# Optimization experiments

Hardware: AMD Instinct MI355X
Metric: run time of the kernel (lower is better)

Reference implementation:

```python
import jax, jax.numpy as jnp
import numpy as np

ACT_BIT = 3
W_BIT = 2


def fake_quant(x, bits):
    """Symmetric uniform fake-quantization to `bits` bits (dequantized values)."""
    qmax = float((1 << (bits - 1)) - 1)
    scale = jnp.max(jnp.abs(x)) / qmax
    scale = jnp.where(scale == 0, jnp.ones_like(scale), scale)
    return jnp.clip(jnp.round(x / scale), -qmax, qmax) * scale


def setup_inputs() -> dict:
    key = jax.random.key(0)
    kA, kX, kWi, kWo = jax.random.split(key, 4)
    N, D_IN, D_H, D_OUT = 8192, 128, 64, 16
    A = jax.random.normal(kA, (N, N), dtype=jnp.float32)       # dense subgraph adjacency (binarized inside)
    X = jax.random.normal(kX, (N, D_IN), dtype=jnp.float32)    # node features
    W_in = jax.random.normal(kWi, (D_IN, D_H), dtype=jnp.float32)
    W_out = jax.random.normal(kWo, (D_H, D_OUT), dtype=jnp.float32)
    return {"A": A, "X": X, "W_in": W_in, "W_out": W_out}


def reference(A, X, W_in, W_out):
    # QGTC GCNConv_Qnt: A quantized to 1 bit, activations to act_bit, weights to w_bit.
    Aq = (A > 0).astype(A.dtype)                 # 1-bit adjacency (bit_qnt(A, 1))
    Xq = fake_quant(X, ACT_BIT)                  # X_Qnt
    Wi = fake_quant(W_in, W_BIT)                 # weight_Qnt
    Wo = fake_quant(W_out, W_BIT)
    # Layer 1: mm_v1(X, W_in) then mm_v1(A, .) with output re-quantized to act_bit
    h = Aq @ (Xq @ Wi)                           # [N, D_H]
    hq = fake_quant(h, ACT_BIT)
    # Layer 2 (output layer)
    out = Aq @ (hq @ Wo)                         # [N, D_OUT]
    return out
```

## Files before the change

### kernel.cpp

```cpp
#include <hip/hip_runtime.h>

#define NN 8192
#define DIN 128
#define DH 64
#define DOUT 16
#define KS 16

typedef _Float16 half8 __attribute__((ext_vector_type(8)));
typedef float f32x4 __attribute__((ext_vector_type(4)));

#define OFF_SC    0u
#define OFF_PART  256u
#define OFF_WIQ   2048u
#define OFF_WOQ   34816u
#define OFF_YT    65536u
#define OFF_RT    1114112u
#define OFF_HF    1376256u
#define OFF_BITS  3473408u
#define OFF_P1    11862016u
#define OFF_P2    45416448u

__device__ __forceinline__ float getscale(const unsigned* sc, int idx, float qmax) {
  float s = __uint_as_float(sc[idx]) / qmax;
  return (s == 0.0f) ? 1.0f : s;
}

__device__ __forceinline__ half8 expand8(unsigned bb) {
  uint4 w;
  w.x = ((bb & 1u)  ? 0x3C00u : 0u) | ((bb & 2u)   ? 0x3C000000u : 0u);
  w.y = ((bb & 4u)  ? 0x3C00u : 0u) | ((bb & 8u)   ? 0x3C000000u : 0u);
  w.z = ((bb & 16u) ? 0x3C00u : 0u) | ((bb & 32u)  ? 0x3C000000u : 0u);
  w.w = ((bb & 64u) ? 0x3C00u : 0u) | ((bb & 128u) ? 0x3C000000u : 0u);
  return __builtin_bit_cast(half8, w);
}

__global__ __launch_bounds__(256) void k_scales(const float* __restrict__ X,
                                                const float* __restrict__ Wi,
                                                const float* __restrict__ Wo,
                                                unsigned* part) {
  __shared__ float red[256];
  int t = threadIdx.x, b = blockIdx.x;
  float m = 0.0f;
  if (b < 240) {
    for (int i = b * 256 + t; i < NN * DIN; i += 240 * 256) m = fmaxf(m, fabsf(X[i]));
  } else if (b == 240) {
    for (int i = t; i < DIN * DH; i += 256) m = fmaxf(m, fabsf(Wi[i]));
  } else {
    for (int i = t; i < DH * DOUT; i += 256) m = fmaxf(m, fabsf(Wo[i]));
  }
  red[t] = m; __syncthreads();
  for (int s = 128; s > 0; s >>= 1) {
    if (t < s) red[t] = fmaxf(red[t], red[t + s]);
    __syncthreads();
  }
  if (t == 0) part[b] = __float_as_uint(red[0]);
}

__global__ __launch_bounds__(256) void k_quantW(const float* __restrict__ Wi,
                                                const float* __restrict__ Wo,
                                                const unsigned* __restrict__ part,
                                                unsigned* sc,
                                                float* __restrict__ Wiq,
                                                float* __restrict__ Woq) {
  __shared__ float red[256];
  int t = threadIdx.x;
  red[t] = (t < 240) ? __uint_as_float(part[t]) : 0.0f;
  __syncthreads();
  for (int s = 128; s > 0; s >>= 1) {
    if (t < s) red[t] = fmaxf(red[t], red[t + s]);
    __syncthreads();
  }
  if (t == 0) {
    sc[0] = __float_as_uint(red[0]);
    sc[1] = part[240];
    sc[2] = part[241];
    sc[3] = 0u;
  }
  float swi = __uint_as_float(part[240]); swi = (swi == 0.0f) ? 1.0f : swi;
  float swo = __uint_as_float(part[241]); swo = (swo == 0.0f) ? 1.0f : swo;
  for (int i = t; i < DIN * DH; i += 256) {
    float q = rintf(Wi[i] / swi);
    Wiq[i] = fminf(fmaxf(q, -1.0f), 1.0f);
  }
  for (int i = t; i < DH * DOUT; i += 256) {
    float q = rintf(Wo[i] / swo);
    Woq[i] = fminf(fmaxf(q, -1.0f), 1.0f);
  }
}

__global__ __launch_bounds__(256) void k_bitsY(const float* __restrict__ A,
                                               const float* __restrict__ X,
                                               const float* __restrict__ Wiq,
                                               const unsigned* __restrict__ sc,
                                               unsigned char* __restrict__ bits,
                                               _Float16* __restrict__ YT) {
  __shared__ float Xs[8][129];
  __shared__ float Ws[DIN][DH];
  const int t = threadIdx.x, bx = blockIdx.x;
  if (bx < 4096) {
    const int g = bx * 256 + t;
    const float4* ap = (const float4*)(A + (size_t)g * 64);
    float4 v[16];
#pragma unroll
    for (int u = 0; u < 16; ++u) v[u] = ap[u];
    unsigned lo = 0u, hi = 0u;
#pragma unroll
    for (int u = 0; u < 8; ++u) {
      lo |= ((unsigned)(v[u].x > 0.0f) << (4 * u + 0)) | ((unsigned)(v[u].y > 0.0f) << (4 * u + 1)) |
            ((unsigned)(v[u].z > 0.0f) << (4 * u + 2)) | ((unsigned)(v[u].w > 0.0f) << (4 * u + 3));
      float4 w = v[u + 8];
      hi |= ((unsigned)(w.x > 0.0f) << (4 * u + 0)) | ((unsigned)(w.y > 0.0f) << (4 * u + 1)) |
            ((unsigned)(w.z > 0.0f) << (4 * u + 2)) | ((unsigned)(w.w > 0.0f) << (4 * u + 3));
    }
    uint2 bw; bw.x = lo; bw.y = hi;
    *(uint2*)(bits + (size_t)g * 8) = bw;
    return;
  }
  float sx = getscale(sc, 0, 3.0f);
  const int by = bx - 4096;
  const int k0 = by * 8;
  for (int i = t; i < 8 * DIN; i += 256) {
    int r = i >> 7, c = i & 127;
    float q = rintf(X[(size_t)(k0 + r) * DIN + c] / sx);
    Xs[r][c] = fminf(fmaxf(q, -3.0f), 3.0f);
  }
  for (int i = t; i < DIN * DH; i += 256) Ws[i >> 6][i & 63] = Wiq[i];
  __syncthreads();
  const int r = t & 7, jp = t >> 3, j = jp * 2;
  float a0 = 0.0f, a1 = 0.0f;
  for (int n = 0; n < DIN; ++n) {
    float xv = Xs[r][n];
    a0 = fmaf(xv, Ws[n][j], a0);
    a1 = fmaf(xv, Ws[n][j + 1], a1);
  }
  YT[(size_t)j * NN + k0 + r]       = (_Float16)a0;
  YT[(size_t)(j + 1) * NN + k0 + r] = (_Float16)a1;
}

__global__ __launch_bounds__(256) void k_gemm1(const unsigned char* __restrict__ bits,
                                               const _Float16* __restrict__ YT,
                                               float* __restrict__ P1) {
  __shared__ __align__(16) char Bs[64 * 128];
  const int t = threadIdx.x, lane = t & 63, warp = t >> 6;
  const int wm = warp >> 1, wn = warp & 1;
  const int row0 = blockIdx.x * 64;
  const int split = blockIdx.y;
  const int l15 = lane & 15, lq = lane >> 4;
  const int sh8 = lq * 8;

  f32x4 acc[2][2] = {};

  const int bn = t >> 2, bp = t & 3;
  const _Float16* bsrc = YT + (size_t)bn * NN + split * 512 + bp * 16;
  char* bdst0 = &Bs[bn * 128 + ((bp * 32) ^ ((bn & 7) << 4))];
  char* bdst1 = &Bs[bn * 128 + ((bp * 32 + 16) ^ ((bn & 7) << 4))];

  const unsigned char* brow0 = bits + (size_t)(row0 + wm * 32 + l15) * 1024 + split * 64;
  const unsigned char* brow1 = brow0 + 16 * 1024;

  uint4 breg0 = *(const uint4*)(bsrc);
  uint4 breg1 = *(const uint4*)(bsrc + 8);

  for (int it = 0; it < 8; ++it) {
    __syncthreads();
    *(uint4*)bdst0 = breg0;
    *(uint4*)bdst1 = breg1;
    if (it < 7) {
      breg0 = *(const uint4*)(bsrc + (it + 1) * 64);
      breg1 = *(const uint4*)(bsrc + (it + 1) * 64 + 8);
    }
    uint2 w0 = *(const uint2*)(brow0 + it * 8);
    uint2 w1 = *(const uint2*)(brow1 + it * 8);
    __syncthreads();
#pragma unroll
    for (int kk = 0; kk < 2; ++kk) {
      half8 af0 = expand8(((kk ? w0.y : w0.x) >> sh8) & 0xffu);
      half8 af1 = expand8(((kk ? w1.y : w1.x) >> sh8) & 0xffu);
#pragma unroll
      for (int n = 0; n < 2; ++n) {
        half8 bf = *(const half8*)(&Bs[(wn * 32 + n * 16 + l15) * 128 +
                                       ((lq * 16 + kk * 64) ^ ((l15 & 7) << 4))]);
        acc[0][n] = __builtin_amdgcn_mfma_f32_16x16x32_f16(af0, bf, acc[0][n], 0, 0, 0);
        acc[1][n] = __builtin_amdgcn_mfma_f32_16x16x32_f16(af1, bf, acc[1][n], 0, 0, 0);
      }
    }
  }
  const int r4 = lq * 4;
#pragma unroll
  for (int mf = 0; mf < 2; ++mf) {
#pragma unroll
    for (int n = 0; n < 2; ++n) {
#pragma unroll
      for (int i = 0; i < 4; ++i) {
        int rr = row0 + wm * 32 + mf * 16 + r4 + i;
        int cc = wn * 32 + n * 16 + l15;
        P1[((size_t)split * NN + rr) * DH + cc] = acc[mf][n][i];
      }
    }
  }
}

__global__ __launch_bounds__(256) void k_h2(const float* __restrict__ P1,
                                            unsigned* sc, float* __restrict__ hf) {
  float sxw = getscale(sc, 0, 3.0f) * getscale(sc, 1, 1.0f);
  int idx = blockIdx.x * 256 + threadIdx.x;
  const float4* p = (const float4*)P1;
  float4 s = {0, 0, 0, 0};
#pragma unroll
  for (int sp = 0; sp < KS; ++sp) {
    float4 v = p[(size_t)sp * (NN * DH / 4) + idx];
    s.x += v.x; s.y += v.y; s.z += v.z; s.w += v.w;
  }
  s.x *= sxw; s.y *= sxw; s.z *= sxw; s.w *= sxw;
  ((float4*)hf)[idx] = s;
  float m = fmaxf(fmaxf(fabsf(s.x), fabsf(s.y)), fmaxf(fabsf(s.z), fabsf(s.w)));
  __shared__ float red[256];
  red[threadIdx.x] = m; __syncthreads();
  for (int st = 128; st > 0; st >>= 1) {
    if (threadIdx.x < st) red[threadIdx.x] = fmaxf(red[threadIdx.x], red[threadIdx.x + st]);
    __syncthreads();
  }
  if (threadIdx.x == 0) atomicMax(&sc[3], __float_as_uint(red[0]));
}

__global__ __launch_bounds__(256) void k_R(const float* __restrict__ hf,
                                           const float* __restrict__ Woq,
                                           const unsigned* __restrict__ sc,
                                           _Float16* __restrict__ RT) {
  __shared__ float WoS[DH][DOUT];
  float sh = getscale(sc, 3, 3.0f);
  int t = threadIdx.x;
  for (int i = t; i < DH * DOUT; i += 256) WoS[i >> 4][i & 15] = Woq[i];
  __syncthreads();
  int i = blockIdx.x * 16 + (t & 15), j = t >> 4;
  const float4* hp = (const float4*)(hf + (size_t)i * DH);
  float acc = 0.0f;
#pragma unroll 4
  for (int nb = 0; nb < 16; ++nb) {
    float4 h4 = hp[nb];
    float q;
    q = fminf(fmaxf(rintf(h4.x / sh), -3.0f), 3.0f); acc = fmaf(q, WoS[nb * 4 + 0][j], acc);
    q = fminf(fmaxf(rintf(h4.y / sh), -3.0f), 3.0f); acc = fmaf(q, WoS[nb * 4 + 1][j], acc);
    q = fminf(fmaxf(rintf(h4.z / sh), -3.0f), 3.0f); acc = fmaf(q, WoS[nb * 4 + 2][j], acc);
    q = fminf(fmaxf(rintf(h4.w / sh), -3.0f), 3.0f); acc = fmaf(q, WoS[nb * 4 + 3][j], acc);
  }
  RT[(size_t)j * NN + i] = (_Float16)acc;
}

__global__ __launch_bounds__(256) void k_gemm2(const unsigned char* __restrict__ bits,
                                               const _Float16* __restrict__ RT,
                                               float* __restrict__ P2) {
  __shared__ __align__(16) char Rs[16 * 1024];
  const int t = threadIdx.x, lane = t & 63, warp = t >> 6;
  const int row0 = blockIdx.x * 64;
  const int split = blockIdx.y;
  const int l15 = lane & 15, lq = lane >> 4;
  const int sh8 = lq * 8;

  {
    const int rr = t >> 4, cb = (t & 15) * 64;
    const uint4* src = (const uint4*)(RT + (size_t)rr * NN + split * 512 + (t & 15) * 32);
    char* base = &Rs[rr * 1024];
    const int sw = (rr & 7) << 4;
#pragma unroll
    for (int u = 0; u < 4; ++u) *(uint4*)(&base[(cb + u * 16) ^ sw]) = src[u];
  }
  __syncthreads();

  const unsigned char* brow = bits + (size_t)(row0 + warp * 16 + l15) * 1024 + split * 64;
  f32x4 acc = {};
  const int rsw = (l15 & 7) << 4;
#pragma unroll
  for (int it = 0; it < 8; ++it) {
    uint2 w = *(const uint2*)(brow + it * 8);
#pragma unroll
    for (int kk = 0; kk < 2; ++kk) {
      half8 af = expand8(((kk ? w.y : w.x) >> sh8) & 0xffu);
      half8 bf = *(const half8*)(&Rs[l15 * 1024 + ((it * 128 + lq * 16 + kk * 64) ^ rsw)]);
      acc = __builtin_amdgcn_mfma_f32_16x16x32_f16(af, bf, acc, 0, 0, 0);
    }
  }
  const int r4 = lq * 4;
#pragma unroll
  for (int i = 0; i < 4; ++i) {
    int rr = row0 + warp * 16 + r4 + i;
    P2[((size_t)split * NN + rr) * DOUT + l15] = acc[i];
  }
}

__global__ __launch_bounds__(256) void k_out(const float* __restrict__ P2,
                                             const unsigned* __restrict__ sc,
                                             float* __restrict__ out) {
  float s = getscale(sc, 3, 3.0f) * getscale(sc, 2, 1.0f);
  int idx = blockIdx.x * 256 + threadIdx.x;
  const float4* p = (const float4*)P2;
  float4 acc = {0, 0, 0, 0};
#pragma unroll
  for (int sp = 0; sp < KS; ++sp) {
    float4 v = p[(size_t)sp * (NN * DOUT / 4) + idx];
    acc.x += v.x; acc.y += v.y; acc.z += v.z; acc.w += v.w;
  }
  acc.x *= s; acc.y *= s; acc.z *= s; acc.w *= s;
  ((float4*)out)[idx] = acc;
}

extern "C" void kernel_launch(void* const* d_in, const int* in_sizes, int n_in,
                              void* d_out, int out_size, void* d_ws, size_t ws_size,
                              hipStream_t stream) {
  const float* A  = (const float*)d_in[0];
  const float* X  = (const float*)d_in[1];
  const float* Wi = (const float*)d_in[2];
  const float* Wo = (const float*)d_in[3];
  char* ws = (char*)d_ws;
  unsigned* sc        = (unsigned*)(ws + OFF_SC);
  unsigned* part      = (unsigned*)(ws + OFF_PART);
  float* Wiq          = (float*)(ws + OFF_WIQ);
  float* Woq          = (float*)(ws + OFF_WOQ);
  _Float16* YT        = (_Float16*)(ws + OFF_YT);
  _Float16* RT        = (_Float16*)(ws + OFF_RT);
  float* hf           = (float*)(ws + OFF_HF);
  unsigned char* bits = (unsigned char*)(ws + OFF_BITS);
  float* P1           = (float*)(ws + OFF_P1);
  float* P2           = (float*)(ws + OFF_P2);
  float* out          = (float*)d_out;

  k_scales<<<242, 256, 0, stream>>>(X, Wi, Wo, part);
  k_quantW<<<1, 256, 0, stream>>>(Wi, Wo, part, sc, Wiq, Woq);
  k_bitsY<<<5120, 256, 0, stream>>>(A, X, Wiq, sc, bits, YT);
  k_gemm1<<<dim3(NN / 64, KS), 256, 0, stream>>>(bits, YT, P1);
  k_h2<<<NN * DH / 1024, 256, 0, stream>>>(P1, sc, hf);
  k_R<<<NN / 16, 256, 0, stream>>>(hf, Woq, sc, RT);
  k_gemm2<<<dim3(NN / 64, KS), 256, 0, stream>>>(bits, RT, P2);
  k_out<<<NN * DOUT / 1024, 256, 0, stream>>>(P2, sc, out);
}
```

Before: 147.2 us.

## Coalesce adjacency bit-packing with wave ballots and widen gemm1 row tile

```diff
diff --git a/kernel.cpp b/kernel.cpp
--- a/kernel.cpp
+++ b/kernel.cpp
@@ -98,22 +98,39 @@
   __shared__ float Ws[DIN][DH];
   const int t = threadIdx.x, bx = blockIdx.x;
   if (bx < 4096) {
-    const int g = bx * 256 + t;
-    const float4* ap = (const float4*)(A + (size_t)g * 64);
-    float4 v[16];
-#pragma unroll
-    for (int u = 0; u < 16; ++u) v[u] = ap[u];
-    unsigned lo = 0u, hi = 0u;
-#pragma unroll
-    for (int u = 0; u < 8; ++u) {
-      lo |= ((unsigned)(v[u].x > 0.0f) << (4 * u + 0)) | ((unsigned)(v[u].y > 0.0f) << (4 * u + 1)) |
-            ((unsigned)(v[u].z > 0.0f) << (4 * u + 2)) | ((unsigned)(v[u].w > 0.0f) << (4 * u + 3));
-      float4 w = v[u + 8];
-      hi |= ((unsigned)(w.x > 0.0f) << (4 * u + 0)) | ((unsigned)(w.y > 0.0f) << (4 * u + 1)) |
-            ((unsigned)(w.z > 0.0f) << (4 * u + 2)) | ((unsigned)(w.w > 0.0f) << (4 * u + 3));
-    }
-    uint2 bw; bw.x = lo; bw.y = hi;
-    *(uint2*)(bits + (size_t)g * 8) = bw;
+    const int lane = t & 63, warp = t >> 6;
+    const size_t wbase = ((size_t)bx * 4 + warp) * 4096;
+    const float* ap = A + wbase + lane;
+    unsigned char* bp = bits + (wbase >> 3);
+    const int l8 = lane & 7;
+#pragma unroll
+    for (int g = 0; g < 8; ++g) {
+      float x0 = ap[g * 512 + 0 * 64];
+      float x1 = ap[g * 512 + 1 * 64];
+      float x2 = ap[g * 512 + 2 * 64];
+      float x3 = ap[g * 512 + 3 * 64];
+      float x4 = ap[g * 512 + 4 * 64];
+      float x5 = ap[g * 512 + 5 * 64];
+      float x6 = ap[g * 512 + 6 * 64];
+      float x7 = ap[g * 512 + 7 * 64];
+      unsigned long long m0 = __ballot(x0 > 0.0f);
+      unsigned long long m1 = __ballot(x1 > 0.0f);
+      unsigned long long m2 = __ballot(x2 > 0.0f);
+      unsigned long long m3 = __ballot(x3 > 0.0f);
+      unsigned long long m4 = __ballot(x4 > 0.0f);
+      unsigned long long m5 = __ballot(x5 > 0.0f);
+      unsigned long long m6 = __ballot(x6 > 0.0f);
+      unsigned long long m7 = __ballot(x7 > 0.0f);
+      unsigned long long mine = m0;
+      mine = (l8 == 1) ? m1 : mine;
+      mine = (l8 == 2) ? m2 : mine;
+      mine = (l8 == 3) ? m3 : mine;
+      mine = (l8 == 4) ? m4 : mine;
+      mine = (l8 == 5) ? m5 : mine;
+      mine = (l8 == 6) ? m6 : mine;
+      mine = (l8 == 7) ? m7 : mine;
+      if (lane < 8) *(unsigned long long*)(bp + g * 64 + l8 * 8) = mine;
+    }
     return;
   }
   float sx = getscale(sc, 0, 3.0f);
@@ -142,20 +159,19 @@
                                                float* __restrict__ P1) {
   __shared__ __align__(16) char Bs[64 * 128];
   const int t = threadIdx.x, lane = t & 63, warp = t >> 6;
-  const int wm = warp >> 1, wn = warp & 1;
-  const int row0 = blockIdx.x * 64;
+  const int row0 = blockIdx.x * 128;
   const int split = blockIdx.y;
   const int l15 = lane & 15, lq = lane >> 4;
   const int sh8 = lq * 8;
 
-  f32x4 acc[2][2] = {};
+  f32x4 acc[2][4] = {};
 
   const int bn = t >> 2, bp = t & 3;
   const _Float16* bsrc = YT + (size_t)bn * NN + split * 512 + bp * 16;
   char* bdst0 = &Bs[bn * 128 + ((bp * 32) ^ ((bn & 7) << 4))];
   char* bdst1 = &Bs[bn * 128 + ((bp * 32 + 16) ^ ((bn & 7) << 4))];
 
-  const unsigned char* brow0 = bits + (size_t)(row0 + wm * 32 + l15) * 1024 + split * 64;
+  const unsigned char* brow0 = bits + (size_t)(row0 + warp * 32 + l15) * 1024 + split * 64;
   const unsigned char* brow1 = brow0 + 16 * 1024;
 
   uint4 breg0 = *(const uint4*)(bsrc);
@@ -177,8 +193,8 @@
       half8 af0 = expand8(((kk ? w0.y : w0.x) >> sh8) & 0xffu);
       half8 af1 = expand8(((kk ? w1.y : w1.x) >> sh8) & 0xffu);
 #pragma unroll
-      for (int n = 0; n < 2; ++n) {
-        half8 bf = *(const half8*)(&Bs[(wn * 32 + n * 16 + l15) * 128 +
+      for (int n = 0; n < 4; ++n) {
+        half8 bf = *(const half8*)(&Bs[(n * 16 + l15) * 128 +
                                        ((lq * 16 + kk * 64) ^ ((l15 & 7) << 4))]);
         acc[0][n] = __builtin_amdgcn_mfma_f32_16x16x32_f16(af0, bf, acc[0][n], 0, 0, 0);
         acc[1][n] = __builtin_amdgcn_mfma_f32_16x16x32_f16(af1, bf, acc[1][n], 0, 0, 0);
@@ -189,11 +205,11 @@
 #pragma unroll
   for (int mf = 0; mf < 2; ++mf) {
 #pragma unroll
-    for (int n = 0; n < 2; ++n) {
+    for (int n = 0; n < 4; ++n) {
 #pragma unroll
       for (int i = 0; i < 4; ++i) {
-        int rr = row0 + wm * 32 + mf * 16 + r4 + i;
-        int cc = wn * 32 + n * 16 + l15;
+        int rr = row0 + warp * 32 + mf * 16 + r4 + i;
+        int cc = n * 16 + l15;
         P1[((size_t)split * NN + rr) * DH + cc] = acc[mf][n][i];
       }
     }
@@ -327,7 +343,7 @@
   k_scales<<<242, 256, 0, stream>>>(X, Wi, Wo, part);
   k_quantW<<<1, 256, 0, stream>>>(Wi, Wo, part, sc, Wiq, Woq);
   k_bitsY<<<5120, 256, 0, stream>>>(A, X, Wiq, sc, bits, YT);
-  k_gemm1<<<dim3(NN / 64, KS), 256, 0, stream>>>(bits, YT, P1);
+  k_gemm1<<<dim3(NN / 128, KS), 256, 0, stream>>>(bits, YT, P1);
   k_h2<<<NN * DH / 1024, 256, 0, stream>>>(P1, sc, hf);
   k_R<<<NN / 16, 256, 0, stream>>>(hf, Woq, sc, RT);
   k_gemm2<<<dim3(NN / 64, KS), 256, 0, stream>>>(bits, RT, P2);
```

Result: faster. 129.9 us (-11.7%).
